# Kernel optimization log

Hardware: AMD Instinct MI355X
Metric: run time of the kernel (lower is better)

Reference implementation:

```python
import jax, jax.numpy as jnp
import numpy as np

B = 65536        # batch of (Z, N) token pairs
V = 512          # vocab size per input
D = 1024         # hidden_dim == embedding_dim
IN = 2 * D       # input_dim = embedding_dim * len(vocab_size)
E = 4            # num_experts (hardcoded in MoEModel)
OUT = 128        # output_dim


def setup_inputs() -> dict:
    key = jax.random.key(0)
    ks = jax.random.split(key, 6)
    x = jax.random.randint(ks[0], (B, 2), 0, V, dtype=jnp.int64)
    emb0 = jax.random.normal(ks[1], (V, D), dtype=jnp.float32)
    emb1 = jax.random.normal(ks[2], (V, D), dtype=jnp.float32)
    W1 = jax.random.normal(ks[3], (E, IN, D), dtype=jnp.float32) * 0.02
    b1 = jnp.zeros((E, D), dtype=jnp.float32)
    W2 = jax.random.normal(ks[4], (E, D, OUT), dtype=jnp.float32) * 0.02
    b2 = jnp.zeros((E, OUT), dtype=jnp.float32)
    Wg = jax.random.normal(ks[5], (IN, E), dtype=jnp.float32) * 0.02
    bg = jnp.zeros((E,), dtype=jnp.float32)
    return {"x": x, "emb0": emb0, "emb1": emb1, "W1": W1, "b1": b1,
            "W2": W2, "b2": b2, "Wg": Wg, "bg": bg}


def reference(x, emb0, emb1, W1, b1, W2, b2, Wg, bg):
    # embed_input: gather each column's embedding and concat -> [B, IN]
    e = jnp.concatenate([emb0[x[:, 0]], emb1[x[:, 1]]], axis=1)
    # gating network: softmax(MuReadout(e)) -> [B, E]
    gates = jax.nn.softmax(e @ Wg + bg, axis=-1)
    # all 4 experts run densely: Linear -> SiLU -> MuReadout, batched over E
    h = jax.nn.silu(jnp.einsum('bi,eid->bed', e, W1) + b1)      # [B, E, D]
    expert_out = jnp.einsum('bed,edo->beo', h, W2) + b2          # [B, E, OUT]
    # einsum('ij,ikj->ik') combine: softmax-weighted mixture over experts
    out = jnp.einsum('be,beo->bo', gates, expert_out)            # [B, OUT]
    return out
```

## Files before the change

kernel.cpp:

```cpp
#include <hip/hip_runtime.h>


typedef __attribute__((ext_vector_type(8))) short short8;
typedef __attribute__((ext_vector_type(4))) float f32x4;

static __device__ __forceinline__ unsigned short f2b(float f) {
  unsigned int u = __builtin_bit_cast(unsigned int, f);
  u += 0x7fffu + ((u >> 16) & 1u);
  return (unsigned short)(u >> 16);
}
static __device__ __forceinline__ float bflo(unsigned int u) {
  return __builtin_bit_cast(float, u << 16);
}
static __device__ __forceinline__ float bfhi(unsigned int u) {
  return __builtin_bit_cast(float, u & 0xffff0000u);
}
static __device__ __forceinline__ unsigned int cvtpk(float a, float b) {
  unsigned int r;
  asm("v_cvt_pk_bf16_f32 %0, %1, %2" : "=v"(r) : "v"(a), "v"(b));
  return r;
}

#define BARRIER() do { asm volatile("s_waitcnt lgkmcnt(0)" ::: "memory"); \
                       __builtin_amdgcn_s_barrier(); } while (0)

__global__ void prep_all(const float* __restrict__ emb0, const float* __restrict__ emb1,
                         const float* __restrict__ Wg, const float* __restrict__ bg,
                         const float* __restrict__ W2, const float* __restrict__ W1,
                         float* __restrict__ G0, float* __restrict__ G1,
                         unsigned short* __restrict__ E0, unsigned short* __restrict__ E1,
                         unsigned short* __restrict__ W2T, unsigned short* __restrict__ W1T) {
  __shared__ __align__(16) char sm[16640];
  const int bid = blockIdx.x;
  const int tid = threadIdx.x;
  if (bid < 1024) {
    float (*red)[256] = (float(*)[256])sm;
    const int half = bid >> 9, v = bid & 511;
    const float* __restrict__ emb = half ? emb1 : emb0;
    const float* __restrict__ wg = Wg + (size_t)half * 1024 * 4;
    float a0 = 0.f, a1 = 0.f, a2 = 0.f, a3 = 0.f;
    for (int i = tid; i < 1024; i += 256) {
      const float ev = emb[(size_t)v * 1024 + i];
      const float4 w = *(const float4*)(wg + (size_t)i * 4);
      a0 += ev * w.x; a1 += ev * w.y; a2 += ev * w.z; a3 += ev * w.w;
    }
    red[0][tid] = a0; red[1][tid] = a1; red[2][tid] = a2; red[3][tid] = a3;
    __syncthreads();
    for (int s = 128; s > 0; s >>= 1) {
      if (tid < s) {
        red[0][tid] += red[0][tid + s]; red[1][tid] += red[1][tid + s];
        red[2][tid] += red[2][tid + s]; red[3][tid] += red[3][tid + s];
      }
      __syncthreads();
    }
    if (tid < 4) {
      const float val = red[tid][0] + (half == 0 ? bg[tid] : 0.f);
      (half ? G1 : G0)[(size_t)v * 4 + tid] = val;
    }
  } else if (bid < 1536) {
    const int idx = bid - 1024;
    const int half = idx >> 8, blk = idx & 255;
    const float* __restrict__ src = half ? emb1 : emb0;
    unsigned short* __restrict__ dst = half ? E1 : E0;
    const size_t base = (size_t)blk * 2048 + (size_t)tid * 8;
    const float4 lo = *(const float4*)(src + base);
    const float4 hi = *(const float4*)(src + base + 4);
    uint4 o;
    o.x = cvtpk(lo.x, lo.y); o.y = cvtpk(lo.z, lo.w);
    o.z = cvtpk(hi.x, hi.y); o.w = cvtpk(hi.z, hi.w);
    *(uint4*)(dst + base) = o;
  } else if (bid < 1664) {
    float (*st)[65] = (float(*)[65])sm;
    const int idx = bid - 1536;
    const int kt = idx & 63, ot = idx >> 6;
    for (int it = 0; it < 16; ++it) {
      const int i2 = it * 256 + tid;
      const int k = i2 >> 6, o = i2 & 63;
      st[k][o] = W2[(size_t)(kt * 64 + k) * 128 + ot * 64 + o];
    }
    __syncthreads();
    for (int it = 0; it < 4; ++it) {
      const int i2 = it * 256 + tid;
      const int o = i2 >> 4, c = i2 & 15;
      const unsigned int p0 = cvtpk(st[c * 4 + 0][o], st[c * 4 + 1][o]);
      const unsigned int p1 = cvtpk(st[c * 4 + 2][o], st[c * 4 + 3][o]);
      *(uint2*)(W2T + (size_t)(ot * 64 + o) * 4096 + kt * 64 + c * 4) = make_uint2(p0, p1);
    }
  } else {
    float (*st)[65] = (float(*)[65])sm;
    const int idx = bid - 1664;
    const int z = idx >> 8, xx = idx & 255;
    const int kt = xx >> 4, dt = xx & 15;
    const int e = z >> 1, half = z & 1;
    const int r = tid >> 2, cg = (tid & 3) * 16;
    const float* src = W1 + ((size_t)e * 2048 + half * 1024 + kt * 64 + r) * 1024 + dt * 64 + cg;
#pragma unroll
    for (int j = 0; j < 4; ++j) {
      const float4 v = *(const float4*)(src + j * 4);
      st[r][cg + j * 4 + 0] = v.x; st[r][cg + j * 4 + 1] = v.y;
      st[r][cg + j * 4 + 2] = v.z; st[r][cg + j * 4 + 3] = v.w;
    }
    __syncthreads();
    const int dr = tid >> 2, kb = (tid & 3) * 16;
    uint4 o0, o1;
    o0.x = cvtpk(st[kb + 0][dr], st[kb + 1][dr]);
    o0.y = cvtpk(st[kb + 2][dr], st[kb + 3][dr]);
    o0.z = cvtpk(st[kb + 4][dr], st[kb + 5][dr]);
    o0.w = cvtpk(st[kb + 6][dr], st[kb + 7][dr]);
    o1.x = cvtpk(st[kb + 8][dr], st[kb + 9][dr]);
    o1.y = cvtpk(st[kb + 10][dr], st[kb + 11][dr]);
    o1.z = cvtpk(st[kb + 12][dr], st[kb + 13][dr]);
    o1.w = cvtpk(st[kb + 14][dr], st[kb + 15][dr]);
    unsigned short* dst = W1T + ((size_t)z * 1024 + dt * 64 + dr) * 1024 + kt * 64 + kb;
    *(uint4*)dst = o0;
    *(uint4*)(dst + 8) = o1;
  }
}

__launch_bounds__(256, 4)
__global__ void build_tables(const unsigned short* __restrict__ E0,
                             const unsigned short* __restrict__ E1,
                             const unsigned short* __restrict__ W1T,
                             const float* __restrict__ b1,
                             unsigned short* __restrict__ T0, unsigned short* __restrict__ T1) {
  __shared__ __align__(16) unsigned short At[64 * 64];
  __shared__ __align__(16) unsigned short Bt[64 * 64];

  const int bid = blockIdx.x;
  const int z = bid >> 7, rem = bid & 127;
  const int vt = rem >> 4, dt = rem & 15;
  const int e = z >> 1, half = z & 1;
  const unsigned short* __restrict__ E = half ? E1 : E0;
  const unsigned short* __restrict__ Wp = W1T + (size_t)z * 1024 * 1024;
  unsigned short* __restrict__ Tout = (half ? T1 : T0) + (size_t)e * 512 * 1024;

  const int tid = threadIdx.x, lane = tid & 63, wave = tid >> 6;
  const int wm = wave >> 1, wn = wave & 1;

  const int arow = tid >> 2, ac = tid & 3;
  int wOff[2];
#pragma unroll
  for (int i = 0; i < 2; ++i)
    wOff[i] = arow * 128 + ((ac * 32 + i * 16) ^ ((arow & 7) << 4));
  const unsigned short* aSrc = E + (size_t)(vt * 64 + arow) * 1024 + ac * 16;
  const unsigned short* bSrc = Wp + (size_t)(dt * 64 + arow) * 1024 + ac * 16;

  const int kq = (lane >> 4) * 16;
  int rAoff[2], rAsw[2], rBoff[2], rBsw[2];
#pragma unroll
  for (int mi = 0; mi < 2; ++mi) {
    const int ra = wm * 32 + mi * 16 + (lane & 15);
    rAoff[mi] = ra * 128; rAsw[mi] = (ra & 7) << 4;
    const int cb = wn * 32 + mi * 16 + (lane & 15);
    rBoff[mi] = cb * 128; rBsw[mi] = (cb & 7) << 4;
  }

  f32x4 acc[2][2] = {};
  uint4 eaA[2], ebA[2], eaB[2], ebB[2];

  auto issue = [&](int kt, uint4* ea, uint4* eb) {
    const int k0 = kt * 64;
    ea[0] = *(const uint4*)(aSrc + k0); ea[1] = *(const uint4*)(aSrc + k0 + 8);
    eb[0] = *(const uint4*)(bSrc + k0); eb[1] = *(const uint4*)(bSrc + k0 + 8);
  };
  auto mfmaStep = [&]() {
#pragma unroll
    for (int kk = 0; kk < 2; ++kk) {
      const int kb = kk * 64 + kq;
      short8 af[2], bfr[2];
#pragma unroll
      for (int mi = 0; mi < 2; ++mi)
        af[mi] = *(const short8*)((char*)At + rAoff[mi] + (kb ^ rAsw[mi]));
#pragma unroll
      for (int ni = 0; ni < 2; ++ni)
        bfr[ni] = *(const short8*)((char*)Bt + rBoff[ni] + (kb ^ rBsw[ni]));
#pragma unroll
      for (int mi = 0; mi < 2; ++mi)
#pragma unroll
        for (int ni = 0; ni < 2; ++ni)
          acc[mi][ni] = __builtin_amdgcn_mfma_f32_16x16x32_bf16(af[mi], bfr[ni], acc[mi][ni], 0, 0, 0);
    }
  };

  issue(0, eaA, ebA);
  issue(1, eaB, ebB);
  for (int kt = 0; kt < 16; kt += 2) {
    BARRIER();
#pragma unroll
    for (int i = 0; i < 2; ++i) {
      *(uint4*)((char*)At + wOff[i]) = eaA[i];
      *(uint4*)((char*)Bt + wOff[i]) = ebA[i];
    }
    if (kt + 2 < 16) issue(kt + 2, eaA, ebA);
    BARRIER();
    __builtin_amdgcn_s_setprio(1);
    mfmaStep();
    __builtin_amdgcn_s_setprio(0);
    BARRIER();
#pragma unroll
    for (int i = 0; i < 2; ++i) {
      *(uint4*)((char*)At + wOff[i]) = eaB[i];
      *(uint4*)((char*)Bt + wOff[i]) = ebB[i];
    }
    if (kt + 3 < 16) issue(kt + 3, eaB, ebB);
    BARRIER();
    __builtin_amdgcn_s_setprio(1);
    mfmaStep();
    __builtin_amdgcn_s_setprio(0);
  }

  const float* bb = b1 + (size_t)e * 1024;
  unsigned short* fs = At;
  BARRIER();
#pragma unroll
  for (int ni = 0; ni < 2; ++ni) {
    const int lc = wn * 32 + ni * 16 + (lane & 15);
    const float bias = (half == 0) ? bb[dt * 64 + lc] : 0.f;
#pragma unroll
    for (int mi = 0; mi < 2; ++mi) {
      const int r0 = wm * 32 + mi * 16 + ((lane >> 4) << 2);
      const f32x4 a = acc[mi][ni];
#pragma unroll
      for (int j = 0; j < 4; ++j) fs[(r0 + j) * 64 + lc] = f2b(a[j] + bias);
    }
  }
  BARRIER();
  {
    const int r = tid >> 2, c = (tid & 3) * 16;
    const uint4 w0 = *(const uint4*)(fs + r * 64 + c);
    const uint4 w1 = *(const uint4*)(fs + r * 64 + c + 8);
    unsigned short* op = Tout + (size_t)(vt * 64 + r) * 1024 + dt * 64 + c;
    *(uint4*)op = w0;
    *(uint4*)(op + 8) = w1;
  }
}

__launch_bounds__(512, 4)
__global__ void moe_main(const int* __restrict__ X,
                         const unsigned short* __restrict__ T0,
                         const unsigned short* __restrict__ T1,
                         const unsigned short* __restrict__ W2T,
                         const float* __restrict__ G0,
                         const float* __restrict__ G1,
                         const float* __restrict__ b2v,
                         float* __restrict__ out) {
  __shared__ __align__(16) char smem[35840];
  unsigned short* At = (unsigned short*)smem;
  unsigned short* Bt = (unsigned short*)(smem + 16384);
  float* gl = (float*)(smem + 32768);
  int* xs0 = (int*)(smem + 34816);
  int* xs1 = (int*)(smem + 35328);

  const int tid = threadIdx.x, lane = tid & 63, wave = tid >> 6;
  const int wm = wave >> 1, wn = wave & 1;
  int bid = blockIdx.x;
  bid = (bid & 7) * 64 + (bid >> 3);
  const int b0 = bid * 128;

  if (tid < 128) {
    const int b = b0 + tid;
    const int x0 = X[2 * b], x1 = X[2 * b + 1];
    xs0[tid] = x0; xs1[tid] = x1;
    const float4 l0 = *(const float4*)(G0 + 4 * x0);
    const float4 l1 = *(const float4*)(G1 + 4 * x1);
    const float z0 = l0.x + l1.x, z1 = l0.y + l1.y;
    const float z2 = l0.z + l1.z, z3 = l0.w + l1.w;
    const float m = fmaxf(fmaxf(z0, z1), fmaxf(z2, z3));
    const float e0 = __expf(z0 - m), e1 = __expf(z1 - m);
    const float e2 = __expf(z2 - m), e3 = __expf(z3 - m);
    const float inv = __builtin_amdgcn_rcpf(e0 + e1 + e2 + e3);
    *(float4*)(&gl[4 * tid]) = make_float4(e0 * inv, e1 * inv, e2 * inv, e3 * inv);
  }
  __syncthreads();

  const int arow = tid >> 2, ac = tid & 3;
  const int sx0 = xs0[arow], sx1 = xs1[arow];
  const float4 grow = *(const float4*)(&gl[4 * arow]);
  int wOff[2];
#pragma unroll
  for (int i = 0; i < 2; ++i)
    wOff[i] = arow * 128 + ((ac * 32 + i * 16) ^ ((arow & 7) << 4));

  const int kq = (lane >> 4) * 16;
  int rAoff[2], rAsw[2], rBoff[4], rBsw[4];
#pragma unroll
  for (int mi = 0; mi < 2; ++mi) {
    const int ra = wm * 32 + mi * 16 + (lane & 15);
    rAoff[mi] = ra * 128; rAsw[mi] = (ra & 7) << 4;
  }
#pragma unroll
  for (int ni = 0; ni < 4; ++ni) {
    const int cb = wn * 64 + ni * 16 + (lane & 15);
    rBoff[ni] = cb * 128; rBsw[ni] = (cb & 7) << 4;
  }

  f32x4 acc[2][4] = {};
  uint4 uaA[2], ubA[2], uaB[2], ubB[2], bw[2];

  auto issueA = [&](int t, uint4* ua, uint4* ub) {
    const int e = t >> 4, d0 = (t & 15) << 6;
    const unsigned short* p0 = T0 + (((size_t)(e * 512 + sx0)) << 10) + d0 + ac * 16;
    const unsigned short* p1 = T1 + (((size_t)(e * 512 + sx1)) << 10) + d0 + ac * 16;
    ua[0] = *(const uint4*)p0; ua[1] = *(const uint4*)(p0 + 8);
    ub[0] = *(const uint4*)p1; ub[1] = *(const uint4*)(p1 + 8);
  };
  auto issueB = [&](int t) {
    const unsigned short* pb = W2T + (size_t)arow * 4096 + t * 64 + ac * 16;
    bw[0] = *(const uint4*)pb; bw[1] = *(const uint4*)(pb + 8);
  };
  auto siluPack = [&](const uint4* ua, const uint4* ub, float g, uint4* sw) {
#pragma unroll
    for (int i = 0; i < 2; ++i) {
      const unsigned int uu[4] = {ua[i].x, ua[i].y, ua[i].z, ua[i].w};
      const unsigned int vv[4] = {ub[i].x, ub[i].y, ub[i].z, ub[i].w};
      unsigned int w[4];
#pragma unroll
      for (int p = 0; p < 4; ++p) {
        const float f0 = bflo(uu[p]) + bflo(vv[p]);
        const float f1 = bfhi(uu[p]) + bfhi(vv[p]);
        const float s0 = g * f0 * __builtin_amdgcn_rcpf(1.f + __expf(-f0));
        const float s1 = g * f1 * __builtin_amdgcn_rcpf(1.f + __expf(-f1));
        w[p] = cvtpk(s0, s1);
      }
      sw[i] = uint4{w[0], w[1], w[2], w[3]};
    }
  };
  auto mfmaStep = [&]() {
#pragma unroll
    for (int kk = 0; kk < 2; ++kk) {
      const int kb = kk * 64 + kq;
      short8 af[2], bfr[4];
#pragma unroll
      for (int mi = 0; mi < 2; ++mi)
        af[mi] = *(const short8*)((char*)At + rAoff[mi] + (kb ^ rAsw[mi]));
#pragma unroll
      for (int ni = 0; ni < 4; ++ni)
        bfr[ni] = *(const short8*)((char*)Bt + rBoff[ni] + (kb ^ rBsw[ni]));
#pragma unroll
      for (int mi = 0; mi < 2; ++mi)
#pragma unroll
        for (int ni = 0; ni < 4; ++ni)
          acc[mi][ni] = __builtin_amdgcn_mfma_f32_16x16x32_bf16(af[mi], bfr[ni], acc[mi][ni], 0, 0, 0);
    }
  };
  auto gsel = [&](int t) -> float {
    const int e = t >> 4;
    return (e == 0) ? grow.x : (e == 1) ? grow.y : (e == 2) ? grow.z : grow.w;
  };

  issueA(0, uaA, ubA);
  issueB(0);
  issueA(1, uaB, ubB);

  for (int t = 0; t < 64; t += 2) {
    {
      uint4 sw[2];
      siluPack(uaA, ubA, gsel(t), sw);
      BARRIER();
      *(uint4*)((char*)At + wOff[0]) = sw[0];
      *(uint4*)((char*)At + wOff[1]) = sw[1];
      *(uint4*)((char*)Bt + wOff[0]) = bw[0];
      *(uint4*)((char*)Bt + wOff[1]) = bw[1];
      if (t + 2 < 64) issueA(t + 2, uaA, ubA);
      issueB(t + 1);
      BARRIER();
      __builtin_amdgcn_s_setprio(1);
      mfmaStep();
      __builtin_amdgcn_s_setprio(0);
    }
    {
      uint4 sw[2];
      siluPack(uaB, ubB, gsel(t + 1), sw);
      BARRIER();
      *(uint4*)((char*)At + wOff[0]) = sw[0];
      *(uint4*)((char*)At + wOff[1]) = sw[1];
      *(uint4*)((char*)Bt + wOff[0]) = bw[0];
      *(uint4*)((char*)Bt + wOff[1]) = bw[1];
      if (t + 3 < 64) { issueA(t + 3, uaB, ubB); issueB(t + 2); }
      BARRIER();
      __builtin_amdgcn_s_setprio(1);
      mfmaStep();
      __builtin_amdgcn_s_setprio(0);
    }
  }

#pragma unroll
  for (int ni = 0; ni < 4; ++ni) {
    const int col = wn * 64 + ni * 16 + (lane & 15);
    const float c0 = b2v[col], c1 = b2v[128 + col];
    const float c2 = b2v[256 + col], c3 = b2v[384 + col];
#pragma unroll
    for (int mi = 0; mi < 2; ++mi) {
#pragma unroll
      for (int j = 0; j < 4; ++j) {
        const int row = wm * 32 + mi * 16 + ((lane >> 4) << 2) + j;
        const float4 g = *(const float4*)(&gl[4 * row]);
        acc[mi][ni][j] += g.x * c0 + g.y * c1 + g.z * c2 + g.w * c3;
      }
    }
  }
  float* fs = (float*)smem;
#pragma unroll
  for (int p = 0; p < 2; ++p) {
    BARRIER();
    if ((wm >> 1) == p) {
      const int rbase = (wm & 1) * 32;
#pragma unroll
      for (int ni = 0; ni < 4; ++ni) {
        const int col = wn * 64 + ni * 16 + (lane & 15);
#pragma unroll
        for (int mi = 0; mi < 2; ++mi) {
          const int r0 = rbase + mi * 16 + ((lane >> 4) << 2);
          const f32x4 a = acc[mi][ni];
#pragma unroll
          for (int j = 0; j < 4; ++j) fs[(r0 + j) * 128 + col] = a[j];
        }
      }
    }
    BARRIER();
    const int r = tid >> 3, c0 = (tid & 7) * 16;
    const float4 v0 = *(const float4*)(fs + r * 128 + c0);
    const float4 v1 = *(const float4*)(fs + r * 128 + c0 + 4);
    const float4 v2 = *(const float4*)(fs + r * 128 + c0 + 8);
    const float4 v3 = *(const float4*)(fs + r * 128 + c0 + 12);
    float* op = out + (size_t)(b0 + p * 64 + r) * 128 + c0;
    *(float4*)op = v0;
    *(float4*)(op + 4) = v1;
    *(float4*)(op + 8) = v2;
    *(float4*)(op + 12) = v3;
  }
}

extern "C" void kernel_launch(void* const* d_in, const int* in_sizes, int n_in,
                              void* d_out, int out_size, void* d_ws, size_t ws_size,
                              hipStream_t stream) {
  const int*   X    = (const int*)  d_in[0];
  const float* emb0 = (const float*)d_in[1];
  const float* emb1 = (const float*)d_in[2];
  const float* W1   = (const float*)d_in[3];
  const float* b1   = (const float*)d_in[4];
  const float* W2   = (const float*)d_in[5];
  const float* b2   = (const float*)d_in[6];
  const float* Wg   = (const float*)d_in[7];
  const float* bg   = (const float*)d_in[8];
  float* out = (float*)d_out;

  char* ws = (char*)d_ws;
  const size_t MB = 1024 * 1024;
  unsigned short* T0  = (unsigned short*)(ws);
  unsigned short* T1  = (unsigned short*)(ws + 4 * MB);
  unsigned short* W2T = (unsigned short*)(ws + 8 * MB);
  float* G0 = (float*)(ws + 9 * MB);
  float* G1 = (float*)(ws + 9 * MB + 8192);
  unsigned short* E0  = (unsigned short*)(ws + 10 * MB);
  unsigned short* E1  = (unsigned short*)(ws + 11 * MB);
  unsigned short* W1T = (unsigned short*)(ws + 12 * MB);

  hipLaunchKernelGGL(prep_all, dim3(3712), dim3(256), 0, stream,
                     emb0, emb1, Wg, bg, W2, W1, G0, G1, E0, E1, W2T, W1T);
  hipLaunchKernelGGL(build_tables, dim3(1024), dim3(256), 0, stream, E0, E1, W1T, b1, T0, T1);
  hipLaunchKernelGGL(moe_main, dim3(512), dim3(512), 0, stream, X, T0, T1, W2T, G0, G1, b2, out);
}
```

Measured before the change: 387.5 us.

## Shrink moe_main tile to 64 rows with 256 threads and single-buffer pipelines

The main MoE kernel drops from 128-row blocks of 512 threads to 64-row blocks of 256 threads, doubling the grid to 1024 blocks and cutting LDS use. Each thread now loads 64 bytes of the W2 tile instead of 32, and the epilogue stores through a padded row stride of 132 floats. The two-deep register double-buffering and s_setprio hints are removed in both moe_main and build_tables, leaving a single prefetch stage. The intent is more resident blocks and less register pressure. The cost is less W2 reuse per block and less latency hiding per wave.

```diff
diff --git a/kernel.cpp b/kernel.cpp
--- a/kernel.cpp
+++ b/kernel.cpp
@@ -156,12 +156,12 @@
   }
 
   f32x4 acc[2][2] = {};
-  uint4 eaA[2], ebA[2], eaB[2], ebB[2];
-
-  auto issue = [&](int kt, uint4* ea, uint4* eb) {
+  uint4 eaA[2], ebA[2];
+
+  auto issue = [&](int kt) {
     const int k0 = kt * 64;
-    ea[0] = *(const uint4*)(aSrc + k0); ea[1] = *(const uint4*)(aSrc + k0 + 8);
-    eb[0] = *(const uint4*)(bSrc + k0); eb[1] = *(const uint4*)(bSrc + k0 + 8);
+    eaA[0] = *(const uint4*)(aSrc + k0); eaA[1] = *(const uint4*)(aSrc + k0 + 8);
+    ebA[0] = *(const uint4*)(bSrc + k0); ebA[1] = *(const uint4*)(bSrc + k0 + 8);
   };
   auto mfmaStep = [&]() {
 #pragma unroll
@@ -182,31 +182,17 @@
     }
   };
 
-  issue(0, eaA, ebA);
-  issue(1, eaB, ebB);
-  for (int kt = 0; kt < 16; kt += 2) {
+  issue(0);
+  for (int kt = 0; kt < 16; ++kt) {
     BARRIER();
 #pragma unroll
     for (int i = 0; i < 2; ++i) {
       *(uint4*)((char*)At + wOff[i]) = eaA[i];
       *(uint4*)((char*)Bt + wOff[i]) = ebA[i];
     }
-    if (kt + 2 < 16) issue(kt + 2, eaA, ebA);
-    BARRIER();
-    __builtin_amdgcn_s_setprio(1);
+    if (kt < 15) issue(kt + 1);
+    BARRIER();
     mfmaStep();
-    __builtin_amdgcn_s_setprio(0);
-    BARRIER();
-#pragma unroll
-    for (int i = 0; i < 2; ++i) {
-      *(uint4*)((char*)At + wOff[i]) = eaB[i];
-      *(uint4*)((char*)Bt + wOff[i]) = ebB[i];
-    }
-    if (kt + 3 < 16) issue(kt + 3, eaB, ebB);
-    BARRIER();
-    __builtin_amdgcn_s_setprio(1);
-    mfmaStep();
-    __builtin_amdgcn_s_setprio(0);
   }
 
   const float* bb = b1 + (size_t)e * 1024;
@@ -235,7 +221,7 @@
   }
 }
 
-__launch_bounds__(512, 4)
+__launch_bounds__(256, 4)
 __global__ void moe_main(const int* __restrict__ X,
                          const unsigned short* __restrict__ T0,
                          const unsigned short* __restrict__ T1,
@@ -244,20 +230,20 @@
                          const float* __restrict__ G1,
                          const float* __restrict__ b2v,
                          float* __restrict__ out) {
-  __shared__ __align__(16) char smem[35840];
+  __shared__ __align__(16) char smem[26112];
   unsigned short* At = (unsigned short*)smem;
-  unsigned short* Bt = (unsigned short*)(smem + 16384);
-  float* gl = (float*)(smem + 32768);
-  int* xs0 = (int*)(smem + 34816);
-  int* xs1 = (int*)(smem + 35328);
+  unsigned short* Bt = (unsigned short*)(smem + 8192);
+  float* gl = (float*)(smem + 24576);
+  int* xs0 = (int*)(smem + 25600);
+  int* xs1 = (int*)(smem + 25856);
 
   const int tid = threadIdx.x, lane = tid & 63, wave = tid >> 6;
   const int wm = wave >> 1, wn = wave & 1;
   int bid = blockIdx.x;
-  bid = (bid & 7) * 64 + (bid >> 3);
-  const int b0 = bid * 128;
-
-  if (tid < 128) {
+  bid = (bid & 7) * 128 + (bid >> 3);
+  const int b0 = bid * 64;
+
+  if (tid < 64) {
     const int b = b0 + tid;
     const int x0 = X[2 * b], x1 = X[2 * b + 1];
     xs0[tid] = x0; xs1[tid] = x1;
@@ -276,10 +262,15 @@
   const int arow = tid >> 2, ac = tid & 3;
   const int sx0 = xs0[arow], sx1 = xs1[arow];
   const float4 grow = *(const float4*)(&gl[4 * arow]);
-  int wOff[2];
+  int wOffA[2];
 #pragma unroll
   for (int i = 0; i < 2; ++i)
-    wOff[i] = arow * 128 + ((ac * 32 + i * 16) ^ ((arow & 7) << 4));
+    wOffA[i] = arow * 128 + ((ac * 32 + i * 16) ^ ((arow & 7) << 4));
+  const int brow = tid >> 1, bc = tid & 1;
+  int wOffB[4];
+#pragma unroll
+  for (int i = 0; i < 4; ++i)
+    wOffB[i] = brow * 128 + ((bc * 64 + i * 16) ^ ((brow & 7) << 4));
 
   const int kq = (lane >> 4) * 16;
   int rAoff[2], rAsw[2], rBoff[4], rBsw[4];
@@ -295,9 +286,9 @@
   }
 
   f32x4 acc[2][4] = {};
-  uint4 uaA[2], ubA[2], uaB[2], ubB[2], bw[2];
-
-  auto issueA = [&](int t, uint4* ua, uint4* ub) {
+  uint4 ua[2], ub[2], bw[4];
+
+  auto issueA = [&](int t) {
     const int e = t >> 4, d0 = (t & 15) << 6;
     const unsigned short* p0 = T0 + (((size_t)(e * 512 + sx0)) << 10) + d0 + ac * 16;
     const unsigned short* p1 = T1 + (((size_t)(e * 512 + sx1)) << 10) + d0 + ac * 16;
@@ -305,10 +296,11 @@
     ub[0] = *(const uint4*)p1; ub[1] = *(const uint4*)(p1 + 8);
   };
   auto issueB = [&](int t) {
-    const unsigned short* pb = W2T + (size_t)arow * 4096 + t * 64 + ac * 16;
-    bw[0] = *(const uint4*)pb; bw[1] = *(const uint4*)(pb + 8);
-  };
-  auto siluPack = [&](const uint4* ua, const uint4* ub, float g, uint4* sw) {
+    const unsigned short* pb = W2T + (size_t)brow * 4096 + t * 64 + bc * 32;
+#pragma unroll
+    for (int i = 0; i < 4; ++i) bw[i] = *(const uint4*)(pb + i * 8);
+  };
+  auto siluPack = [&](float g, uint4* sw) {
 #pragma unroll
     for (int i = 0; i < 2; ++i) {
       const unsigned int uu[4] = {ua[i].x, ua[i].y, ua[i].z, ua[i].w};
@@ -348,40 +340,20 @@
     return (e == 0) ? grow.x : (e == 1) ? grow.y : (e == 2) ? grow.z : grow.w;
   };
 
-  issueA(0, uaA, ubA);
+  issueA(0);
   issueB(0);
-  issueA(1, uaB, ubB);
-
-  for (int t = 0; t < 64; t += 2) {
-    {
-      uint4 sw[2];
-      siluPack(uaA, ubA, gsel(t), sw);
-      BARRIER();
-      *(uint4*)((char*)At + wOff[0]) = sw[0];
-      *(uint4*)((char*)At + wOff[1]) = sw[1];
-      *(uint4*)((char*)Bt + wOff[0]) = bw[0];
-      *(uint4*)((char*)Bt + wOff[1]) = bw[1];
-      if (t + 2 < 64) issueA(t + 2, uaA, ubA);
-      issueB(t + 1);
-      BARRIER();
-      __builtin_amdgcn_s_setprio(1);
-      mfmaStep();
-      __builtin_amdgcn_s_setprio(0);
-    }
-    {
-      uint4 sw[2];
-      siluPack(uaB, ubB, gsel(t + 1), sw);
-      BARRIER();
-      *(uint4*)((char*)At + wOff[0]) = sw[0];
-      *(uint4*)((char*)At + wOff[1]) = sw[1];
-      *(uint4*)((char*)Bt + wOff[0]) = bw[0];
-      *(uint4*)((char*)Bt + wOff[1]) = bw[1];
-      if (t + 3 < 64) { issueA(t + 3, uaB, ubB); issueB(t + 2); }
-      BARRIER();
-      __builtin_amdgcn_s_setprio(1);
-      mfmaStep();
-      __builtin_amdgcn_s_setprio(0);
-    }
+  for (int t = 0; t < 64; ++t) {
+    uint4 sa[2];
+    siluPack(gsel(t), sa);
+    if (t < 63) issueA(t + 1);
+    BARRIER();
+    *(uint4*)((char*)At + wOffA[0]) = sa[0];
+    *(uint4*)((char*)At + wOffA[1]) = sa[1];
+#pragma unroll
+    for (int i = 0; i < 4; ++i) *(uint4*)((char*)Bt + wOffB[i]) = bw[i];
+    if (t < 63) issueB(t + 1);
+    BARRIER();
+    mfmaStep();
   }
 
 #pragma unroll
@@ -403,27 +375,26 @@
 #pragma unroll
   for (int p = 0; p < 2; ++p) {
     BARRIER();
-    if ((wm >> 1) == p) {
-      const int rbase = (wm & 1) * 32;
+    if (wm == p) {
 #pragma unroll
       for (int ni = 0; ni < 4; ++ni) {
         const int col = wn * 64 + ni * 16 + (lane & 15);
 #pragma unroll
         for (int mi = 0; mi < 2; ++mi) {
-          const int r0 = rbase + mi * 16 + ((lane >> 4) << 2);
+          const int r0 = mi * 16 + ((lane >> 4) << 2);
           const f32x4 a = acc[mi][ni];
 #pragma unroll
-          for (int j = 0; j < 4; ++j) fs[(r0 + j) * 128 + col] = a[j];
+          for (int j = 0; j < 4; ++j) fs[(r0 + j) * 132 + col] = a[j];
         }
       }
     }
     BARRIER();
     const int r = tid >> 3, c0 = (tid & 7) * 16;
-    const float4 v0 = *(const float4*)(fs + r * 128 + c0);
-    const float4 v1 = *(const float4*)(fs + r * 128 + c0 + 4);
-    const float4 v2 = *(const float4*)(fs + r * 128 + c0 + 8);
-    const float4 v3 = *(const float4*)(fs + r * 128 + c0 + 12);
-    float* op = out + (size_t)(b0 + p * 64 + r) * 128 + c0;
+    const float4 v0 = *(const float4*)(fs + r * 132 + c0);
+    const float4 v1 = *(const float4*)(fs + r * 132 + c0 + 4);
+    const float4 v2 = *(const float4*)(fs + r * 132 + c0 + 8);
+    const float4 v3 = *(const float4*)(fs + r * 132 + c0 + 12);
+    float* op = out + (size_t)(b0 + p * 32 + r) * 128 + c0;
     *(float4*)op = v0;
     *(float4*)(op + 4) = v1;
     *(float4*)(op + 8) = v2;
@@ -459,5 +430,5 @@
   hipLaunchKernelGGL(prep_all, dim3(3712), dim3(256), 0, stream,
                      emb0, emb1, Wg, bg, W2, W1, G0, G1, E0, E1, W2T, W1T);
   hipLaunchKernelGGL(build_tables, dim3(1024), dim3(256), 0, stream, E0, E1, W1T, b1, T0, T1);
-  hipLaunchKernelGGL(moe_main, dim3(512), dim3(512), 0, stream, X, T0, T1, W2T, G0, G1, b2, out);
-}
+  hipLaunchKernelGGL(moe_main, dim3(1024), dim3(256), 0, stream, X, T0, T1, W2T, G0, G1, b2, out);
+}
```

Measured after the change: 511.4 us. +32.0%, slower.
